# Performance work log

Measured on AMD Instinct MI355X. Metric: run time of the kernel, lower is better.

## Reference

```python
import jax, jax.numpy as jnp
import numpy as np


def setup_inputs() -> dict:
    key = jax.random.key(0)
    k1, k2, k3, k4, k5 = jax.random.split(key, 5)
    B, S, I, O, R = 4, 2048, 4096, 4096, 16
    s = 1.0 / np.sqrt(I)
    return {
        "x": jax.random.normal(k1, (B, S, I), dtype=jnp.float32),
        "W": jax.random.normal(k2, (O, I), dtype=jnp.float32) * s,
        "b": jax.random.normal(k3, (O,), dtype=jnp.float32) * 0.02,
        "lora_A": jax.random.normal(k4, (I, R), dtype=jnp.float32) * s,
        "lora_B": jax.random.normal(k5, (R, O), dtype=jnp.float32) * 0.02,
    }


def reference(x, W, b, lora_A, lora_B):
    # Base linear: F.linear(x, W, b) = x @ W.T + b   -> [B, S, O]
    base_out = jnp.einsum("bsi,oi->bso", x, W) + b
    # LoRA low-rank delta: (x @ A) @ B  -> [B, S, O]
    lora_out = jnp.einsum("bsr,ro->bso", jnp.einsum("bsi,ir->bsr", x, lora_A), lora_B)
    return base_out + lora_out
```

## Files before the change

kernel.cpp:

```cpp
#include <hip/hip_runtime.h>

typedef float f32x4 __attribute__((ext_vector_type(4)));
typedef __bf16 bf16x8 __attribute__((ext_vector_type(8)));
typedef __bf16 bf16x4 __attribute__((ext_vector_type(4)));

#define GLOBAL_AS __attribute__((address_space(1)))
#define LDS_AS    __attribute__((address_space(3)))

static __device__ __forceinline__ void gload16(const void* g, void* l) {
  __builtin_amdgcn_global_load_lds((const GLOBAL_AS void*)g, (LDS_AS void*)l, 16, 0, 0);
}

#define BAR() __builtin_amdgcn_s_barrier()
#define WAITL0() do { asm volatile("s_waitcnt lgkmcnt(0)" ::: "memory"); __builtin_amdgcn_sched_barrier(0); } while (0)

__global__ __launch_bounds__(256)
void prep_all(const float* __restrict__ X, const float* __restrict__ A,
              const float* __restrict__ W, const float* __restrict__ Bl,
              __bf16* __restrict__ Xb, __bf16* __restrict__ XAb,
              __bf16* __restrict__ Wb, __bf16* __restrict__ BlT) {
  __shared__ float Xs[16][68];
  __shared__ float At[16][68];
  const int bid = blockIdx.x;
  const int t = threadIdx.x;
  if (bid < 512) {
    constexpr int K = 4096, KC = 64;
    const int m0 = bid * 16;
    const int lrow = t >> 4, c4 = (t & 15) * 4;
    const int orow = t >> 4, oc = t & 15;
    const int akk = t >> 2, ar4 = (t & 3) * 4;
    f32x4 av = (f32x4)0.f;
    for (int k0 = 0; k0 < K; k0 += KC) {
      f32x4 u = *reinterpret_cast<const f32x4*>(X + (size_t)(m0 + lrow) * K + k0 + c4);
      *reinterpret_cast<f32x4*>(&Xs[lrow][c4]) = u;
      bf16x4 p;
#pragma unroll
      for (int e = 0; e < 4; ++e) p[e] = (__bf16)u[e];
      *reinterpret_cast<bf16x4*>(Xb + (size_t)(m0 + lrow) * K + k0 + c4) = p;
      f32x4 a = *reinterpret_cast<const f32x4*>(A + (size_t)(k0 + akk) * 16 + ar4);
      At[ar4 + 0][akk] = a[0]; At[ar4 + 1][akk] = a[1];
      At[ar4 + 2][akk] = a[2]; At[ar4 + 3][akk] = a[3];
      __syncthreads();
#pragma unroll
      for (int q = 0; q < 16; ++q) {
        f32x4 xv = *reinterpret_cast<const f32x4*>(&Xs[orow][q * 4]);
        av += xv * *reinterpret_cast<const f32x4*>(&At[oc][q * 4]);
      }
      __syncthreads();
    }
    const float acc = av[0] + av[1] + av[2] + av[3];
    const size_t base = (size_t)(m0 + orow) * 64;
    XAb[base + oc] = (__bf16)acc;
#pragma unroll
    for (int z = 0; z < 3; ++z) XAb[base + 16 + z * 16 + oc] = (__bf16)0.f;
  } else if (bid < 1536) {
    long base = (long)(bid - 512) * 256 + t;
#pragma unroll
    for (int r = 0; r < 8; ++r) {
      long i = base + (long)r * 262144;
      f32x4 u = reinterpret_cast<const f32x4*>(W)[2 * i];
      f32x4 v = reinterpret_cast<const f32x4*>(W)[2 * i + 1];
      bf16x8 p;
#pragma unroll
      for (int e = 0; e < 4; ++e) { p[e] = (__bf16)u[e]; p[4 + e] = (__bf16)v[e]; }
      reinterpret_cast<bf16x8*>(Wb)[i] = p;
    }
  } else {
    int idx = (bid - 1536) * 256 + t;
    int col = idx >> 6, k = idx & 63;
    float v = (k < 16) ? Bl[(size_t)k * 4096 + col] : 0.f;
    BlT[idx] = (__bf16)v;
  }
}

__global__ __launch_bounds__(512, 2)
void gemm8(const __bf16* __restrict__ Xb, const __bf16* __restrict__ Wb,
           const __bf16* __restrict__ XAb, const __bf16* __restrict__ BlT,
           const float* __restrict__ bias, float* __restrict__ out) {
  constexpr int N = 4096, K = 4096;
  __shared__ __align__(16) char sm[131072];
  char* Asm_ = sm;
  char* Bsm_ = sm + 65536;

  const int t = threadIdx.x;
  const int lane = t & 63, w = t >> 6;
  const int wr = w >> 2, wc = w & 3;
  const int fr = lane & 15, fg = lane >> 4;

  const int bid = blockIdx.x;
  const int xcd = bid & 7, l = bid >> 3;
  const int mt = (xcd << 2) | ((l >> 4) & 2) | (l & 1);
  const int nt = (l >> 1) & 15;
  const int m0 = mt * 256, n0 = nt * 256;

  const int sRow = w * 16 + (lane >> 2);
  const int sColB = (((lane & 3) ^ ((lane >> 3) & 3)) << 4);
  const int rdOff = fr * 64 + ((fg ^ ((fr >> 1) & 3)) << 4);
  const int rdOffA = wr * 16384 + rdOff;
  const int rdOffB = (wc >> 1) * 16384 + (wc & 1) * 8192 + rdOff;

  const char* gA0 = (const char*)Xb + (size_t)(m0 + sRow) * 8192 + sColB;
  const char* gA1 = (const char*)Xb + (size_t)(m0 + 128 + sRow) * 8192 + sColB;
  const char* gB0 = (const char*)Wb + (size_t)(n0 + sRow) * 8192 + sColB;
  const char* gB1 = (const char*)Wb + (size_t)(n0 + 128 + sRow) * 8192 + sColB;

  auto stage2 = [&](const char* g, char* dst) { gload16(g, dst); gload16(g + 64, dst + 1024); };

  auto rdA = [&](int b, int mf, int kk) -> bf16x8 {
    return *reinterpret_cast<const bf16x8*>(Asm_ + b * 32768 + (mf * 2 + kk) * 1024 + rdOffA);
  };
  auto rdB = [&](int b, int nf, int kk) -> bf16x8 {
    return *reinterpret_cast<const bf16x8*>(Bsm_ + b * 32768 + (nf * 2 + kk) * 1024 + rdOffB);
  };

  f32x4 acc[8][4];
#pragma unroll
  for (int i = 0; i < 8; ++i)
#pragma unroll
    for (int j = 0; j < 4; ++j) acc[i][j] = (f32x4)0.f;

  bf16x8 aF[4][2], bL[2][2], bH[2][2];

  auto MF = [&](bf16x8 (&af)[4][2], bf16x8 (&bf_)[2][2], int mi, int ni) {
#pragma unroll
    for (int i = 0; i < 4; ++i)
#pragma unroll
      for (int j = 0; j < 2; ++j)
#pragma unroll
        for (int kk = 0; kk < 2; ++kk)
          acc[mi * 4 + i][ni * 2 + j] = __builtin_amdgcn_mfma_f32_16x16x32_bf16(
              af[i][kk], bf_[j][kk], acc[mi * 4 + i][ni * 2 + j], 0, 0, 0);
  };

  float bb[4];
#pragma unroll
  for (int j = 0; j < 4; ++j) bb[j] = bias[n0 + wc * 64 + j * 16 + fr];

  stage2(gA0, Asm_ + w * 2048);
  stage2(gA1, Asm_ + 16384 + w * 2048);
  stage2(gB0, Bsm_ + w * 2048);
  stage2(gB1, Bsm_ + 16384 + w * 2048);
  stage2(gB0 + 128, Bsm_ + 32768 + w * 2048);
  stage2(gB1 + 128, Bsm_ + 32768 + 16384 + w * 2048);
  asm volatile("s_waitcnt vmcnt(4)" ::: "memory");
  BAR();

  const char* pA0 = gA0 + 128;
  const char* pA1 = gA1 + 128;
  const char* pB0 = gB0 + 256;
  const char* pB1 = gB1 + 256;

  auto tile_step = [&](int b) {
    char* dstA = Asm_ + (b ^ 1) * 32768 + w * 2048;
    char* dstB = Bsm_ + b * 32768 + w * 2048;
#pragma unroll
    for (int i = 0; i < 4; ++i)
#pragma unroll
      for (int kk = 0; kk < 2; ++kk) aF[i][kk] = rdA(b, i, kk);
#pragma unroll
    for (int j = 0; j < 2; ++j)
#pragma unroll
      for (int kk = 0; kk < 2; ++kk) bL[j][kk] = rdB(b, j, kk);
    stage2(pA0, dstA); pA0 += 128;
    asm volatile("s_waitcnt lgkmcnt(8)" ::: "memory");
    BAR(); WAITL0();
    __builtin_amdgcn_s_setprio(1); MF(aF, bL, 0, 0); __builtin_amdgcn_s_setprio(0);
    BAR();
#pragma unroll
    for (int j = 0; j < 2; ++j)
#pragma unroll
      for (int kk = 0; kk < 2; ++kk) bH[j][kk] = rdB(b, 2 + j, kk);
    stage2(pA1, dstA + 16384); pA1 += 128;
    BAR(); WAITL0();
    __builtin_amdgcn_s_setprio(1); MF(aF, bH, 0, 1); __builtin_amdgcn_s_setprio(0);
    BAR();
#pragma unroll
    for (int i = 0; i < 4; ++i)
#pragma unroll
      for (int kk = 0; kk < 2; ++kk) aF[i][kk] = rdA(b, 4 + i, kk);
    stage2(pB0, dstB); pB0 += 128;
    BAR(); WAITL0();
    __builtin_amdgcn_s_setprio(1); MF(aF, bH, 1, 1); __builtin_amdgcn_s_setprio(0);
    BAR();
    stage2(pB1, dstB + 16384); pB1 += 128;
    BAR(); WAITL0();
    __builtin_amdgcn_s_setprio(1); MF(aF, bL, 1, 0); __builtin_amdgcn_s_setprio(0);
    asm volatile("s_waitcnt vmcnt(4)" ::: "memory");
    BAR();
  };

  for (int tp = 0; tp < 31; ++tp) { tile_step(0); tile_step(1); }

  {
    const char* gBl0 = (const char*)BlT + (size_t)(n0 + sRow) * 128 + sColB;
    const char* gBl1 = (const char*)BlT + (size_t)(n0 + 128 + sRow) * 128 + sColB;
    char* dstA = Asm_ + 32768 + w * 2048;
    char* dstB = Bsm_ + w * 2048;
#pragma unroll
    for (int i = 0; i < 4; ++i)
#pragma unroll
      for (int kk = 0; kk < 2; ++kk) aF[i][kk] = rdA(0, i, kk);
#pragma unroll
    for (int j = 0; j < 2; ++j)
#pragma unroll
      for (int kk = 0; kk < 2; ++kk) bL[j][kk] = rdB(0, j, kk);
    stage2(pA0, dstA);
    asm volatile("s_waitcnt lgkmcnt(8)" ::: "memory");
    BAR(); WAITL0();
    __builtin_amdgcn_s_setprio(1); MF(aF, bL, 0, 0); __builtin_amdgcn_s_setprio(0);
    BAR();
#pragma unroll
    for (int j = 0; j < 2; ++j)
#pragma unroll
      for (int kk = 0; kk < 2; ++kk) bH[j][kk] = rdB(0, 2 + j, kk);
    stage2(pA1, dstA + 16384);
    BAR(); WAITL0();
    __builtin_amdgcn_s_setprio(1); MF(aF, bH, 0, 1); __builtin_amdgcn_s_setprio(0);
    BAR();
#pragma unroll
    for (int i = 0; i < 4; ++i)
#pragma unroll
      for (int kk = 0; kk < 2; ++kk) aF[i][kk] = rdA(0, 4 + i, kk);
    stage2(gBl0, dstB);
    BAR(); WAITL0();
    __builtin_amdgcn_s_setprio(1); MF(aF, bH, 1, 1); __builtin_amdgcn_s_setprio(0);
    BAR();
    stage2(gBl1, dstB + 16384);
    BAR(); WAITL0();
    __builtin_amdgcn_s_setprio(1); MF(aF, bL, 1, 0); __builtin_amdgcn_s_setprio(0);
    asm volatile("s_waitcnt vmcnt(4)" ::: "memory");
    BAR();
  }

  {
    const char* gXA0 = (const char*)XAb + (size_t)(m0 + sRow) * 128 + sColB;
    const char* gXA1 = (const char*)XAb + (size_t)(m0 + 128 + sRow) * 128 + sColB;
    char* dstA = Asm_ + w * 2048;
#pragma unroll
    for (int i = 0; i < 4; ++i)
#pragma unroll
      for (int kk = 0; kk < 2; ++kk) aF[i][kk] = rdA(1, i, kk);
#pragma unroll
    for (int j = 0; j < 2; ++j)
#pragma unroll
      for (int kk = 0; kk < 2; ++kk) bL[j][kk] = rdB(1, j, kk);
    stage2(gXA0, dstA);
    asm volatile("s_waitcnt lgkmcnt(8)" ::: "memory");
    BAR(); WAITL0();
    __builtin_amdgcn_s_setprio(1); MF(aF, bL, 0, 0); __builtin_amdgcn_s_setprio(0);
    BAR();
#pragma unroll
    for (int j = 0; j < 2; ++j)
#pragma unroll
      for (int kk = 0; kk < 2; ++kk) bH[j][kk] = rdB(1, 2 + j, kk);
    stage2(gXA1, dstA + 16384);
    BAR(); WAITL0();
    __builtin_amdgcn_s_setprio(1); MF(aF, bH, 0, 1); __builtin_amdgcn_s_setprio(0);
    BAR();
#pragma unroll
    for (int i = 0; i < 4; ++i)
#pragma unroll
      for (int kk = 0; kk < 2; ++kk) aF[i][kk] = rdA(1, 4 + i, kk);
    BAR(); WAITL0();
    __builtin_amdgcn_s_setprio(1); MF(aF, bH, 1, 1); __builtin_amdgcn_s_setprio(0);
    BAR();
    __builtin_amdgcn_s_setprio(1); MF(aF, bL, 1, 0); __builtin_amdgcn_s_setprio(0);
    BAR();
  }

  asm volatile("s_waitcnt vmcnt(0)" ::: "memory");
  BAR();
  {
#pragma unroll
    for (int i = 0; i < 4; ++i)
#pragma unroll
      for (int kk = 0; kk < 2; ++kk) aF[i][kk] = rdA(0, i, kk);
#pragma unroll
    for (int j = 0; j < 2; ++j)
#pragma unroll
      for (int kk = 0; kk < 2; ++kk) { bL[j][kk] = rdB(0, j, kk); bH[j][kk] = rdB(0, 2 + j, kk); }
    MF(aF, bL, 0, 0); MF(aF, bH, 0, 1);
#pragma unroll
    for (int i = 0; i < 4; ++i)
#pragma unroll
      for (int kk = 0; kk < 2; ++kk) aF[i][kk] = rdA(0, 4 + i, kk);
    MF(aF, bH, 1, 1); MF(aF, bL, 1, 0);
  }

#pragma unroll
  for (int i = 0; i < 8; ++i) {
    const int row0 = m0 + wr * 128 + i * 16 + fg * 4;
#pragma unroll
    for (int j = 0; j < 4; ++j) {
      const int col = n0 + wc * 64 + j * 16 + fr;
#pragma unroll
      for (int q = 0; q < 4; ++q)
        out[(size_t)(row0 + q) * N + col] = acc[i][j][q] + bb[j];
    }
  }
}

extern "C" void kernel_launch(void* const* d_in, const int* in_sizes, int n_in,
                              void* d_out, int out_size, void* d_ws, size_t ws_size,
                              hipStream_t stream) {
  const float* x  = (const float*)d_in[0];
  const float* W  = (const float*)d_in[1];
  const float* b  = (const float*)d_in[2];
  const float* lA = (const float*)d_in[3];
  const float* lB = (const float*)d_in[4];
  float* out = (float*)d_out;

  char* ws = (char*)d_ws;
  __bf16* Xb  = (__bf16*)ws;
  __bf16* Wb  = (__bf16*)(ws + 67108864);
  __bf16* XAb = (__bf16*)(ws + 100663296);
  __bf16* BlT = (__bf16*)(ws + 101711872);

  prep_all<<<2560, 256, 0, stream>>>(x, lA, W, lB, Xb, XAb, Wb, BlT);
  gemm8<<<dim3(512), dim3(512), 0, stream>>>(Xb, Wb, XAb, BlT, b, out);
}
```

Measured before the change: 315.8 us.

## Switch GEMM inner product from 16x16x32 to 32x32x16 bf16 MFMA tiles

Replaces the 16x16x32 MFMA instructions with 32x32x16 ones. The LDS fragment read addressing, the accumulator layout (f32x16 per 32x32 tile) and the output epilogue row and column mapping are reworked to match. The larger MFMA shape is meant to cut instruction count and LDS read traffic per FLOP through better operand reuse. The risk is different register pressure and a more complex swizzled read pattern. A few redundant lgkmcnt waits in the tail stages are also dropped.

```diff
diff --git a/kernel.cpp b/kernel.cpp
--- a/kernel.cpp
+++ b/kernel.cpp
@@ -1,6 +1,7 @@
 #include <hip/hip_runtime.h>
 
 typedef float f32x4 __attribute__((ext_vector_type(4)));
+typedef float f32x16 __attribute__((ext_vector_type(16)));
 typedef __bf16 bf16x8 __attribute__((ext_vector_type(8)));
 typedef __bf16 bf16x4 __attribute__((ext_vector_type(4)));
 
@@ -77,7 +78,7 @@
 void gemm8(const __bf16* __restrict__ Xb, const __bf16* __restrict__ Wb,
            const __bf16* __restrict__ XAb, const __bf16* __restrict__ BlT,
            const float* __restrict__ bias, float* __restrict__ out) {
-  constexpr int N = 4096, K = 4096;
+  constexpr int N = 4096;
   __shared__ __align__(16) char sm[131072];
   char* Asm_ = sm;
   char* Bsm_ = sm + 65536;
@@ -85,7 +86,10 @@
   const int t = threadIdx.x;
   const int lane = t & 63, w = t >> 6;
   const int wr = w >> 2, wc = w & 3;
-  const int fr = lane & 15, fg = lane >> 4;
+  const int fr = lane & 15;
+  const int r31 = lane & 31;
+  const int rHi = r31 >> 4;
+  const int kHalf = lane >> 5;
 
   const int bid = blockIdx.x;
   const int xcd = bid & 7, l = bid >> 3;
@@ -95,9 +99,12 @@
 
   const int sRow = w * 16 + (lane >> 2);
   const int sColB = (((lane & 3) ^ ((lane >> 3) & 3)) << 4);
-  const int rdOff = fr * 64 + ((fg ^ ((fr >> 1) & 3)) << 4);
-  const int rdOffA = wr * 16384 + rdOff;
-  const int rdOffB = (wc >> 1) * 16384 + (wc & 1) * 8192 + rdOff;
+
+  const int swzKey = (fr >> 1) & 3;
+  const int sE = ((kHalf ^ swzKey) << 4);
+  const int sO = sE ^ 32;
+  const int baseA = wr * 16384 + rHi * 2048 + fr * 64;
+  const int baseB = (wc >> 1) * 16384 + (wc & 1) * 8192 + rHi * 2048 + fr * 64;
 
   const char* gA0 = (const char*)Xb + (size_t)(m0 + sRow) * 8192 + sColB;
   const char* gA1 = (const char*)Xb + (size_t)(m0 + 128 + sRow) * 8192 + sColB;
@@ -106,35 +113,35 @@
 
   auto stage2 = [&](const char* g, char* dst) { gload16(g, dst); gload16(g + 64, dst + 1024); };
 
-  auto rdA = [&](int b, int mf, int kk) -> bf16x8 {
-    return *reinterpret_cast<const bf16x8*>(Asm_ + b * 32768 + (mf * 2 + kk) * 1024 + rdOffA);
+  auto rdA32 = [&](int b, int mf, int ks) -> bf16x8 {
+    return *reinterpret_cast<const bf16x8*>(
+        Asm_ + b * 32768 + baseA + mf * 4096 + (ks >> 1) * 1024 + ((ks & 1) ? sO : sE));
   };
-  auto rdB = [&](int b, int nf, int kk) -> bf16x8 {
-    return *reinterpret_cast<const bf16x8*>(Bsm_ + b * 32768 + (nf * 2 + kk) * 1024 + rdOffB);
+  auto rdB32 = [&](int b, int nf, int ks) -> bf16x8 {
+    return *reinterpret_cast<const bf16x8*>(
+        Bsm_ + b * 32768 + baseB + nf * 4096 + (ks >> 1) * 1024 + ((ks & 1) ? sO : sE));
   };
 
-  f32x4 acc[8][4];
-#pragma unroll
-  for (int i = 0; i < 8; ++i)
-#pragma unroll
-    for (int j = 0; j < 4; ++j) acc[i][j] = (f32x4)0.f;
-
-  bf16x8 aF[4][2], bL[2][2], bH[2][2];
-
-  auto MF = [&](bf16x8 (&af)[4][2], bf16x8 (&bf_)[2][2], int mi, int ni) {
-#pragma unroll
-    for (int i = 0; i < 4; ++i)
-#pragma unroll
-      for (int j = 0; j < 2; ++j)
-#pragma unroll
-        for (int kk = 0; kk < 2; ++kk)
-          acc[mi * 4 + i][ni * 2 + j] = __builtin_amdgcn_mfma_f32_16x16x32_bf16(
-              af[i][kk], bf_[j][kk], acc[mi * 4 + i][ni * 2 + j], 0, 0, 0);
+  f32x16 acc[4][2];
+#pragma unroll
+  for (int i = 0; i < 4; ++i)
+#pragma unroll
+    for (int j = 0; j < 2; ++j) acc[i][j] = (f32x16)0.f;
+
+  bf16x8 aF[2][4], bL[4], bH[4];
+
+  auto MF = [&](bf16x8 (&af)[2][4], bf16x8 (&bf_)[4], int mh, int nf) {
+#pragma unroll
+    for (int mi = 0; mi < 2; ++mi)
+#pragma unroll
+      for (int ks = 0; ks < 4; ++ks)
+        acc[mh * 2 + mi][nf] = __builtin_amdgcn_mfma_f32_32x32x16_bf16(
+            af[mi][ks], bf_[ks], acc[mh * 2 + mi][nf], 0, 0, 0);
   };
 
-  float bb[4];
-#pragma unroll
-  for (int j = 0; j < 4; ++j) bb[j] = bias[n0 + wc * 64 + j * 16 + fr];
+  float bb[2];
+#pragma unroll
+  for (int j = 0; j < 2; ++j) bb[j] = bias[n0 + wc * 64 + j * 32 + r31];
 
   stage2(gA0, Asm_ + w * 2048);
   stage2(gA1, Asm_ + 16384 + w * 2048);
@@ -154,30 +161,26 @@
     char* dstA = Asm_ + (b ^ 1) * 32768 + w * 2048;
     char* dstB = Bsm_ + b * 32768 + w * 2048;
 #pragma unroll
-    for (int i = 0; i < 4; ++i)
-#pragma unroll
-      for (int kk = 0; kk < 2; ++kk) aF[i][kk] = rdA(b, i, kk);
-#pragma unroll
-    for (int j = 0; j < 2; ++j)
-#pragma unroll
-      for (int kk = 0; kk < 2; ++kk) bL[j][kk] = rdB(b, j, kk);
+    for (int mi = 0; mi < 2; ++mi)
+#pragma unroll
+      for (int ks = 0; ks < 4; ++ks) aF[mi][ks] = rdA32(b, mi, ks);
+#pragma unroll
+    for (int ks = 0; ks < 4; ++ks) bL[ks] = rdB32(b, 0, ks);
     stage2(pA0, dstA); pA0 += 128;
     asm volatile("s_waitcnt lgkmcnt(8)" ::: "memory");
     BAR(); WAITL0();
     __builtin_amdgcn_s_setprio(1); MF(aF, bL, 0, 0); __builtin_amdgcn_s_setprio(0);
     BAR();
 #pragma unroll
-    for (int j = 0; j < 2; ++j)
-#pragma unroll
-      for (int kk = 0; kk < 2; ++kk) bH[j][kk] = rdB(b, 2 + j, kk);
+    for (int ks = 0; ks < 4; ++ks) bH[ks] = rdB32(b, 1, ks);
     stage2(pA1, dstA + 16384); pA1 += 128;
     BAR(); WAITL0();
     __builtin_amdgcn_s_setprio(1); MF(aF, bH, 0, 1); __builtin_amdgcn_s_setprio(0);
     BAR();
 #pragma unroll
-    for (int i = 0; i < 4; ++i)
-#pragma unroll
-      for (int kk = 0; kk < 2; ++kk) aF[i][kk] = rdA(b, 4 + i, kk);
+    for (int mi = 0; mi < 2; ++mi)
+#pragma unroll
+      for (int ks = 0; ks < 4; ++ks) aF[mi][ks] = rdA32(b, 2 + mi, ks);
     stage2(pB0, dstB); pB0 += 128;
     BAR(); WAITL0();
     __builtin_amdgcn_s_setprio(1); MF(aF, bH, 1, 1); __builtin_amdgcn_s_setprio(0);
@@ -197,30 +200,25 @@
     char* dstA = Asm_ + 32768 + w * 2048;
     char* dstB = Bsm_ + w * 2048;
 #pragma unroll
-    for (int i = 0; i < 4; ++i)
-#pragma unroll
-      for (int kk = 0; kk < 2; ++kk) aF[i][kk] = rdA(0, i, kk);
-#pragma unroll
-    for (int j = 0; j < 2; ++j)
-#pragma unroll
-      for (int kk = 0; kk < 2; ++kk) bL[j][kk] = rdB(0, j, kk);
+    for (int mi = 0; mi < 2; ++mi)
+#pragma unroll
+      for (int ks = 0; ks < 4; ++ks) aF[mi][ks] = rdA32(0, mi, ks);
+#pragma unroll
+    for (int ks = 0; ks < 4; ++ks) bL[ks] = rdB32(0, 0, ks);
     stage2(pA0, dstA);
-    asm volatile("s_waitcnt lgkmcnt(8)" ::: "memory");
     BAR(); WAITL0();
     __builtin_amdgcn_s_setprio(1); MF(aF, bL, 0, 0); __builtin_amdgcn_s_setprio(0);
     BAR();
 #pragma unroll
-    for (int j = 0; j < 2; ++j)
-#pragma unroll
-      for (int kk = 0; kk < 2; ++kk) bH[j][kk] = rdB(0, 2 + j, kk);
+    for (int ks = 0; ks < 4; ++ks) bH[ks] = rdB32(0, 1, ks);
     stage2(pA1, dstA + 16384);
     BAR(); WAITL0();
     __builtin_amdgcn_s_setprio(1); MF(aF, bH, 0, 1); __builtin_amdgcn_s_setprio(0);
     BAR();
 #pragma unroll
-    for (int i = 0; i < 4; ++i)
-#pragma unroll
-      for (int kk = 0; kk < 2; ++kk) aF[i][kk] = rdA(0, 4 + i, kk);
+    for (int mi = 0; mi < 2; ++mi)
+#pragma unroll
+      for (int ks = 0; ks < 4; ++ks) aF[mi][ks] = rdA32(0, 2 + mi, ks);
     stage2(gBl0, dstB);
     BAR(); WAITL0();
     __builtin_amdgcn_s_setprio(1); MF(aF, bH, 1, 1); __builtin_amdgcn_s_setprio(0);
@@ -237,30 +235,25 @@
     const char* gXA1 = (const char*)XAb + (size_t)(m0 + 128 + sRow) * 128 + sColB;
     char* dstA = Asm_ + w * 2048;
 #pragma unroll
-    for (int i = 0; i < 4; ++i)
-#pragma unroll
-      for (int kk = 0; kk < 2; ++kk) aF[i][kk] = rdA(1, i, kk);
-#pragma unroll
-    for (int j = 0; j < 2; ++j)
-#pragma unroll
-      for (int kk = 0; kk < 2; ++kk) bL[j][kk] = rdB(1, j, kk);
+    for (int mi = 0; mi < 2; ++mi)
+#pragma unroll
+      for (int ks = 0; ks < 4; ++ks) aF[mi][ks] = rdA32(1, mi, ks);
+#pragma unroll
+    for (int ks = 0; ks < 4; ++ks) bL[ks] = rdB32(1, 0, ks);
     stage2(gXA0, dstA);
-    asm volatile("s_waitcnt lgkmcnt(8)" ::: "memory");
     BAR(); WAITL0();
     __builtin_amdgcn_s_setprio(1); MF(aF, bL, 0, 0); __builtin_amdgcn_s_setprio(0);
     BAR();
 #pragma unroll
-    for (int j = 0; j < 2; ++j)
-#pragma unroll
-      for (int kk = 0; kk < 2; ++kk) bH[j][kk] = rdB(1, 2 + j, kk);
+    for (int ks = 0; ks < 4; ++ks) bH[ks] = rdB32(1, 1, ks);
     stage2(gXA1, dstA + 16384);
     BAR(); WAITL0();
     __builtin_amdgcn_s_setprio(1); MF(aF, bH, 0, 1); __builtin_amdgcn_s_setprio(0);
     BAR();
 #pragma unroll
-    for (int i = 0; i < 4; ++i)
-#pragma unroll
-      for (int kk = 0; kk < 2; ++kk) aF[i][kk] = rdA(1, 4 + i, kk);
+    for (int mi = 0; mi < 2; ++mi)
+#pragma unroll
+      for (int ks = 0; ks < 4; ++ks) aF[mi][ks] = rdA32(1, 2 + mi, ks);
     BAR(); WAITL0();
     __builtin_amdgcn_s_setprio(1); MF(aF, bH, 1, 1); __builtin_amdgcn_s_setprio(0);
     BAR();
@@ -272,30 +265,30 @@
   BAR();
   {
 #pragma unroll
-    for (int i = 0; i < 4; ++i)
-#pragma unroll
-      for (int kk = 0; kk < 2; ++kk) aF[i][kk] = rdA(0, i, kk);
-#pragma unroll
-    for (int j = 0; j < 2; ++j)
-#pragma unroll
-      for (int kk = 0; kk < 2; ++kk) { bL[j][kk] = rdB(0, j, kk); bH[j][kk] = rdB(0, 2 + j, kk); }
+    for (int mi = 0; mi < 2; ++mi)
+#pragma unroll
+      for (int ks = 0; ks < 4; ++ks) aF[mi][ks] = rdA32(0, mi, ks);
+#pragma unroll
+    for (int ks = 0; ks < 4; ++ks) { bL[ks] = rdB32(0, 0, ks); bH[ks] = rdB32(0, 1, ks); }
     MF(aF, bL, 0, 0); MF(aF, bH, 0, 1);
 #pragma unroll
-    for (int i = 0; i < 4; ++i)
-#pragma unroll
-      for (int kk = 0; kk < 2; ++kk) aF[i][kk] = rdA(0, 4 + i, kk);
+    for (int mi = 0; mi < 2; ++mi)
+#pragma unroll
+      for (int ks = 0; ks < 4; ++ks) aF[mi][ks] = rdA32(0, 2 + mi, ks);
     MF(aF, bH, 1, 1); MF(aF, bL, 1, 0);
   }
 
 #pragma unroll
-  for (int i = 0; i < 8; ++i) {
-    const int row0 = m0 + wr * 128 + i * 16 + fg * 4;
-#pragma unroll
-    for (int j = 0; j < 4; ++j) {
-      const int col = n0 + wc * 64 + j * 16 + fr;
-#pragma unroll
-      for (int q = 0; q < 4; ++q)
-        out[(size_t)(row0 + q) * N + col] = acc[i][j][q] + bb[j];
+  for (int mfb = 0; mfb < 4; ++mfb) {
+#pragma unroll
+    for (int nfb = 0; nfb < 2; ++nfb) {
+      const int col = n0 + wc * 64 + nfb * 32 + r31;
+      const int rbase = m0 + wr * 128 + mfb * 32 + 4 * kHalf;
+#pragma unroll
+      for (int q = 0; q < 16; ++q) {
+        const int row = rbase + (q & 3) + 8 * (q >> 2);
+        out[(size_t)row * N + col] = acc[mfb][nfb][q] + bb[nfb];
+      }
     }
   }
 }
```

New measurement: 349.2 us. 10.6% more time.
